# Kernel optimization log

Measured on AMD Instinct MI355X. Metric: run time of the kernel, lower is better.

The kernel has to match this reference:

```python
import jax, jax.numpy as jnp
import numpy as np

N, E = 50000, 800000
D, H, C, ED = 128, 8, 16, 4  # embed_dim, heads, head_dim, edge_dim


def _add_self_loops(edge_index, ea, n):
    # PyG add_self_loops with fill_value='mean': self-loop edge_attr is the
    # mean of incoming edge attributes per destination node (0 if none).
    src, dst = edge_index[0], edge_index[1]
    deg = jax.ops.segment_sum(jnp.ones((src.shape[0],), ea.dtype), dst, num_segments=n)
    loop_ea = jax.ops.segment_sum(ea, dst, num_segments=n) / jnp.maximum(deg, 1.0)[:, None]
    ar = jnp.arange(n, dtype=src.dtype)
    return (jnp.concatenate([src, ar]), jnp.concatenate([dst, ar]),
            jnp.concatenate([ea, loop_ea], axis=0))


def _gatv2(x, src, dst, ea, Wl, bl, Wr, br, We, att, bias, concat):
    n = x.shape[0]
    xl = (x @ Wl + bl).reshape(n, H, C)   # lin_l -> messages (source)
    xr = (x @ Wr + br).reshape(n, H, C)   # lin_r -> target
    e = (ea @ We).reshape(-1, H, C)       # lin_edge (no bias in PyG)
    m = jax.nn.leaky_relu(xl[src] + xr[dst] + e, negative_slope=0.2)  # [Etot,H,C]
    alpha = jnp.einsum('ehc,hc->eh', m, att)
    amax = jax.ops.segment_max(alpha, dst, num_segments=n)   # every node has a self loop
    ex = jnp.exp(alpha - amax[dst])
    den = jax.ops.segment_sum(ex, dst, num_segments=n)
    a = ex / den[dst]                                        # segment softmax over dst
    out = jax.ops.segment_sum(xl[src] * a[:, :, None], dst, num_segments=n)  # [N,H,C]
    out = out.reshape(n, H * C) if concat else out.mean(axis=1)
    return out + bias


def _ln(h, g, b):
    mu = h.mean(-1, keepdims=True)
    var = jnp.var(h, axis=-1, keepdims=True)
    return (h - mu) / jnp.sqrt(var + 1e-5) * g + b


def setup_inputs() -> dict:
    key = jax.random.key(0)
    ks = jax.random.split(key, 32)
    s = 0.05
    inp = {
        'x': jax.random.normal(ks[0], (N, D), jnp.float32),
        'edge_index': jax.random.randint(ks[1], (2, E), 0, N, jnp.int32),
        'edge_attr': jax.random.normal(ks[2], (E, ED), jnp.float32),
    }
    dims = [(D, H * C), (H * C, H * C), (H * C, C)]  # (in_dim, bias_dim per layer)
    k = 3
    for i, (din, bdim) in enumerate(dims):
        inp[f'Wl{i}'] = jax.random.normal(ks[k], (din, H * C), jnp.float32) * s; k += 1
        inp[f'bl{i}'] = jnp.zeros((H * C,), jnp.float32)
        inp[f'Wr{i}'] = jax.random.normal(ks[k], (din, H * C), jnp.float32) * s; k += 1
        inp[f'br{i}'] = jnp.zeros((H * C,), jnp.float32)
        inp[f'We{i}'] = jax.random.normal(ks[k], (ED, H * C), jnp.float32) * s; k += 1
        inp[f'att{i}'] = jax.random.normal(ks[k], (H, C), jnp.float32) * s; k += 1
        inp[f'b{i}'] = jnp.zeros((bdim,), jnp.float32)
        inp[f'g{i}'] = jnp.ones((bdim,), jnp.float32)
        inp[f'be{i}'] = jnp.zeros((bdim,), jnp.float32)
    inp['Wout'] = jax.random.normal(ks[k], (C, D), jnp.float32) * s
    inp['bout'] = jnp.zeros((D,), jnp.float32)
    return inp


def reference(x, edge_index, edge_attr,
              Wl0, bl0, Wr0, br0, We0, att0, b0, g0, be0,
              Wl1, bl1, Wr1, br1, We1, att1, b1, g1, be1,
              Wl2, bl2, Wr2, br2, We2, att2, b2, g2, be2,
              Wout, bout):
    n = x.shape[0]
    src, dst, ea = _add_self_loops(edge_index, edge_attr, n)
    layers = [
        (Wl0, bl0, Wr0, br0, We0, att0, b0, g0, be0, True),
        (Wl1, bl1, Wr1, br1, We1, att1, b1, g1, be1, True),
        (Wl2, bl2, Wr2, br2, We2, att2, b2, g2, be2, False),
    ]
    for (Wl, bl, Wr, br, We, att, bias, g, be, concat) in layers:
        h = _gatv2(x, src, dst, ea, Wl, bl, Wr, br, We, att, bias, concat)
        h = jax.nn.elu(h)
        h = _ln(h, g, be)
        if h.shape == x.shape:  # residual (layers 0,1)
            h = h + x
        x = h
    return x @ Wout + bout
```

## Files before the change

kernel.cpp:

```cpp
#include <hip/hip_runtime.h>
#include <hip/hip_bf16.h>

#define ND 128
#define NH 8
#define NC 16

typedef float v2f __attribute__((ext_vector_type(2)));

static inline size_t alignup(size_t x){ return (x + 255) & ~size_t(255); }

__device__ __forceinline__ ushort f2bf(float f){
    __hip_bfloat16 h = __float2bfloat16(f);
    return *reinterpret_cast<ushort*>(&h);
}

__device__ __forceinline__ v2f unpack_bf2(uint u){
    v2f r;
    r.x = __uint_as_float(u << 16);
    r.y = __uint_as_float(u & 0xffff0000u);
    return r;
}

__device__ __forceinline__ v2f lrelu2(v2f z){
    v2f s = z * 0.2f;
    v2f r;
    r.x = fmaxf(z.x, s.x);
    r.y = fmaxf(z.y, s.y);
    return r;
}

__device__ __forceinline__ float hred8(float x){
    int y;
    y = __builtin_amdgcn_mov_dpp(__float_as_int(x), 0xB1, 0xF, 0xF, true);
    x += __int_as_float(y);
    y = __builtin_amdgcn_mov_dpp(__float_as_int(x), 0x4E, 0xF, 0xF, true);
    x += __int_as_float(y);
    y = __builtin_amdgcn_mov_dpp(__float_as_int(x), 0x141, 0xF, 0xF, true);
    x += __int_as_float(y);
    return x;
}


__global__ void hist_kernel(const int* __restrict__ dsts, int* __restrict__ deg, int E)
{
    int e = blockIdx.x * blockDim.x + threadIdx.x;
    if (e >= E) return;
    atomicAdd(&deg[dsts[e]], 1);
}

__global__ __launch_bounds__(1024) void scan_kernel(const int* __restrict__ deg,
                                                    int* __restrict__ rowstart, int n)
{
    __shared__ int wsum[16];
    int tid = threadIdx.x;
    int lane = tid & 63, wid = tid >> 6;
    int carry = 0;
    for (int base = 0; base < n; base += 4096) {
        int idx = base + tid * 4;
        int4 d = make_int4(0, 0, 0, 0);
        if (idx + 3 < n) d = *(const int4*)(deg + idx);
        else {
            if (idx < n)     d.x = deg[idx];
            if (idx + 1 < n) d.y = deg[idx + 1];
            if (idx + 2 < n) d.z = deg[idx + 2];
        }
        int p0 = (d.x + 3) & ~3, p1 = (d.y + 3) & ~3;
        int p2 = (d.z + 3) & ~3, p3 = (d.w + 3) & ~3;
        int tsum = p0 + p1 + p2 + p3;
        int s = tsum;
        #pragma unroll
        for (int o = 1; o < 64; o <<= 1) {
            int t = __shfl_up(s, o);
            if (lane >= o) s += t;
        }
        if (lane == 63) wsum[wid] = s;
        __syncthreads();
        int off = carry;
        #pragma unroll
        for (int w = 0; w < 16; ++w) {
            int ws_ = wsum[w];
            if (w < wid) off += ws_;
        }
        int total = 0;
        #pragma unroll
        for (int w = 0; w < 16; ++w) total += wsum[w];
        int excl = off + (s - tsum);
        if (idx < n)     rowstart[idx]     = excl;
        if (idx + 1 < n) rowstart[idx + 1] = excl + p0;
        if (idx + 2 < n) rowstart[idx + 2] = excl + p0 + p1;
        if (idx + 3 < n) rowstart[idx + 3] = excl + p0 + p1 + p2;
        carry += total;
        __syncthreads();
    }
    if (tid == 0) rowstart[n] = carry;
}

__global__ void scatter_kernel(const int* __restrict__ srcs, const int* __restrict__ dsts,
                               const float4* __restrict__ ea4,
                               const int* __restrict__ rowstart, int* __restrict__ cursor,
                               int* __restrict__ srcb_sorted, uint2* __restrict__ eab_sorted, int E)
{
    int e = blockIdx.x * blockDim.x + threadIdx.x;
    if (e >= E) return;
    int d = dsts[e];
    int pos = rowstart[d] + atomicAdd(&cursor[d], 1);
    srcb_sorted[pos] = srcs[e] << 8;
    float4 a = ea4[e];
    uint2 p;
    p.x = (uint)f2bf(a.x) | ((uint)f2bf(a.y) << 16);
    p.y = (uint)f2bf(a.z) | ((uint)f2bf(a.w) << 16);
    eab_sorted[pos] = p;
}

__global__ void padfill_kernel(const int* __restrict__ rowstart, const int* __restrict__ deg,
                               int* __restrict__ srcb_sorted, uint2* __restrict__ eab_sorted, int n)
{
    int v = blockIdx.x * blockDim.x + threadIdx.x;
    if (v < n) {
        int d = deg[v];
        int p = rowstart[v] + d;
        int pe = rowstart[v] + ((d + 3) & ~3);
        for (; p < pe; ++p) {
            srcb_sorted[p] = 0;
            eab_sorted[p] = make_uint2(0u, 0u);
        }
    } else if (v < n + 64) {
        int p = rowstart[n] + (v - n);
        srcb_sorted[p] = 0;
        eab_sorted[p] = make_uint2(0u, 0u);
    }
}

__global__ void easum_kernel(const int* __restrict__ rowstart, const int* __restrict__ deg,
                             const uint2* __restrict__ eab_sorted, float4* __restrict__ easum, int n)
{
    int v = blockIdx.x * blockDim.x + threadIdx.x;
    if (v >= n) return;
    int p0 = rowstart[v], d = deg[v];
    float sx = 0.f, sy = 0.f, sz = 0.f, sw = 0.f;
    for (int p = p0; p < p0 + d; ++p) {
        uint2 a = eab_sorted[p];
        sx += __uint_as_float(a.x << 16);
        sy += __uint_as_float(a.x & 0xffff0000u);
        sz += __uint_as_float(a.y << 16);
        sw += __uint_as_float(a.y & 0xffff0000u);
    }
    float inv = 1.0f / (float)(d > 0 ? d : 1);
    easum[v] = make_float4(sx * inv, sy * inv, sz * inv, sw * inv);
}


__global__ __launch_bounds__(256) void gemm_xw2(const float* __restrict__ X,
                                                const float* __restrict__ Wl,
                                                const float* __restrict__ bl,
                                                const float* __restrict__ Wr,
                                                const float* __restrict__ br,
                                                ushort* __restrict__ XLB,
                                                ushort* __restrict__ XRB, int nrows)
{
    __shared__ float xs[64][128];
    __shared__ float wls[16][128];
    __shared__ float wrs[16][128];
    int tid = threadIdx.x;
    int row0 = blockIdx.x * 64;

    const float4* X4 = (const float4*)X;
    float4* xs4 = (float4*)xs;
    #pragma unroll
    for (int i = tid; i < 64*32; i += 256) {
        int r = i >> 5;
        float4 v = make_float4(0.f, 0.f, 0.f, 0.f);
        if (row0 + r < nrows) v = X4[(size_t)(row0 + r) * 32 + (i & 31)];
        xs4[i] = v;
    }

    const float4* Wl4 = (const float4*)Wl;
    const float4* Wr4 = (const float4*)Wr;
    float4 pa0 = Wl4[tid], pa1 = Wl4[tid + 256];
    float4 pb0 = Wr4[tid], pb1 = Wr4[tid + 256];

    int cg = tid & 31;
    int rg = (tid >> 5) * 8;
    v2f al0[8], al1[8], ar0[8], ar1[8];
    float4 blv = ((const float4*)bl)[cg];
    float4 brv = ((const float4*)br)[cg];
    #pragma unroll
    for (int r = 0; r < 8; r++) {
        al0[r] = (v2f){blv.x, blv.y}; al1[r] = (v2f){blv.z, blv.w};
        ar0[r] = (v2f){brv.x, brv.y}; ar1[r] = (v2f){brv.z, brv.w};
    }

    for (int kt = 0; kt < 128; kt += 16) {
        __syncthreads();
        ((float4*)wls)[tid] = pa0; ((float4*)wls)[tid + 256] = pa1;
        ((float4*)wrs)[tid] = pb0; ((float4*)wrs)[tid + 256] = pb1;
        __syncthreads();
        if (kt + 16 < 128) {
            int base = (kt + 16) * 32;
            pa0 = Wl4[base + tid]; pa1 = Wl4[base + tid + 256];
            pb0 = Wr4[base + tid]; pb1 = Wr4[base + tid + 256];
        }
        #pragma unroll
        for (int kk = 0; kk < 16; kk++) {
            float4 wl = ((const float4*)&wls[kk][0])[cg];
            float4 wr = ((const float4*)&wrs[kk][0])[cg];
            v2f wl01 = (v2f){wl.x, wl.y}, wl23 = (v2f){wl.z, wl.w};
            v2f wr01 = (v2f){wr.x, wr.y}, wr23 = (v2f){wr.z, wr.w};
            #pragma unroll
            for (int r = 0; r < 8; r++) {
                float xv = xs[rg + r][kt + kk];
                v2f xv2 = (v2f){xv, xv};
                al0[r] += xv2 * wl01;
                al1[r] += xv2 * wl23;
                ar0[r] += xv2 * wr01;
                ar1[r] += xv2 * wr23;
            }
        }
    }

    #pragma unroll
    for (int r = 0; r < 8; r++) {
        int row = row0 + rg + r;
        if (row < nrows) {
            ushort4 ol, orr;
            ol.x = f2bf(al0[r].x); ol.y = f2bf(al0[r].y);
            ol.z = f2bf(al1[r].x); ol.w = f2bf(al1[r].y);
            orr.x = f2bf(ar0[r].x); orr.y = f2bf(ar0[r].y);
            orr.z = f2bf(ar1[r].x); orr.w = f2bf(ar1[r].y);
            ((ushort4*)XLB)[(size_t)row * 32 + cg] = ol;
            ((ushort4*)XRB)[(size_t)row * 32 + cg] = orr;
        }
    }
}


__device__ __forceinline__ void gat_wave(
    int dstv, int t,
    const uint* __restrict__ xl_u, const uint* __restrict__ xr_u,
    const int* __restrict__ rowstart, const int* __restrict__ deg,
    const int* __restrict__ srcb_sorted, const uint2* __restrict__ eab_sorted,
    const float4* __restrict__ easum,
    const float* __restrict__ We, const float* __restrict__ att,
    v2f& r_out, float& l_out)
{
    v2f we0  = ((const v2f*)(We))[t];
    v2f we1  = ((const v2f*)(We + ND))[t];
    v2f we2  = ((const v2f*)(We + 2*ND))[t];
    v2f we3  = ((const v2f*)(We + 3*ND))[t];
    v2f attv = ((const v2f*)att)[t] * 1.44269504f;
    v2f xrv  = unpack_bf2(xr_u[(((uint)dstv) << 6) + t]);

    int p0 = __builtin_amdgcn_readfirstlane(rowstart[dstv]);
    int dv = __builtin_amdgcn_readfirstlane(deg[dstv]);
    int nb = (dv + 3) >> 2;

    uint xsw = xl_u[(((uint)dstv) << 6) + t];

    const int* sp = srcb_sorted + p0;
    const uint4* ebp = (const uint4*)(eab_sorted + p0);
    const char* xlc = (const char*)xl_u;
    uint t4 = (uint)t * 4u;

    v2f a = {0.f, 0.f};
    float lsum = 0.f;

    int4 s0 = *(const int4*)(sp);
    uint xA0 = *(const uint*)(xlc + ((uint)s0.x + t4));
    uint xA1 = *(const uint*)(xlc + ((uint)s0.y + t4));
    uint xA2 = *(const uint*)(xlc + ((uint)s0.z + t4));
    uint xA3 = *(const uint*)(xlc + ((uint)s0.w + t4));
    int4 s1 = *(const int4*)(sp + 4);
    uint xB0 = *(const uint*)(xlc + ((uint)s1.x + t4));
    uint xB1 = *(const uint*)(xlc + ((uint)s1.y + t4));
    uint xB2 = *(const uint*)(xlc + ((uint)s1.z + t4));
    uint xB3 = *(const uint*)(xlc + ((uint)s1.w + t4));
    int4 s2 = *(const int4*)(sp + 8);
    uint xC0 = *(const uint*)(xlc + ((uint)s2.x + t4));
    uint xC1 = *(const uint*)(xlc + ((uint)s2.y + t4));
    uint xC2 = *(const uint*)(xlc + ((uint)s2.z + t4));
    uint xC3 = *(const uint*)(xlc + ((uint)s2.w + t4));
    int4 s3 = *(const int4*)(sp + 12);
    uint4 eA = ebp[0];
    uint4 eB = ebp[1];

    for (int ib = 0; ib < nb; ++ib) {
        uint xD0 = *(const uint*)(xlc + ((uint)s3.x + t4));
        uint xD1 = *(const uint*)(xlc + ((uint)s3.y + t4));
        uint xD2 = *(const uint*)(xlc + ((uint)s3.z + t4));
        uint xD3 = *(const uint*)(xlc + ((uint)s3.w + t4));
        int4 s4 = *(const int4*)(sp + ib*4 + 16);
        uint4 eNA = ebp[(ib + 1) * 2];
        uint4 eNB = ebp[(ib + 1) * 2 + 1];

        float e0x = __uint_as_float(eA.x << 16), e0y = __uint_as_float(eA.x & 0xffff0000u);
        float e0z = __uint_as_float(eA.y << 16), e0w = __uint_as_float(eA.y & 0xffff0000u);
        float e1x = __uint_as_float(eA.z << 16), e1y = __uint_as_float(eA.z & 0xffff0000u);
        float e1z = __uint_as_float(eA.w << 16), e1w = __uint_as_float(eA.w & 0xffff0000u);
        float e2x = __uint_as_float(eB.x << 16), e2y = __uint_as_float(eB.x & 0xffff0000u);
        float e2z = __uint_as_float(eB.y << 16), e2w = __uint_as_float(eB.y & 0xffff0000u);
        float e3x = __uint_as_float(eB.z << 16), e3y = __uint_as_float(eB.z & 0xffff0000u);
        float e3z = __uint_as_float(eB.w << 16), e3w = __uint_as_float(eB.w & 0xffff0000u);

        v2f b0 = xrv + we0*e0x + we1*e0y + we2*e0z + we3*e0w;
        v2f b1 = xrv + we0*e1x + we1*e1y + we2*e1z + we3*e1w;
        v2f b2 = xrv + we0*e2x + we1*e2y + we2*e2z + we3*e2w;
        v2f b3 = xrv + we0*e3x + we1*e3y + we2*e3z + we3*e3w;

        v2f x0 = unpack_bf2(xA0);
        v2f x1 = unpack_bf2(xA1);
        v2f x2 = unpack_bf2(xA2);
        v2f x3 = unpack_bf2(xA3);

        v2f l0 = lrelu2(x0 + b0);
        v2f l1 = lrelu2(x1 + b1);
        v2f l2 = lrelu2(x2 + b2);
        v2f l3 = lrelu2(x3 + b3);

        v2f q0 = l0 * attv;
        v2f q1 = l1 * attv;
        v2f q2 = l2 * attv;
        v2f q3 = l3 * attv;
        float pt0 = q0.x + q0.y;
        float pt1 = q1.x + q1.y;
        float pt2 = q2.x + q2.y;
        float pt3 = q3.x + q3.y;

        if (ib == nb - 1) {
            int live = dv - ib*4;
            pt1 = (live > 1) ? pt1 : -1e30f;
            pt2 = (live > 2) ? pt2 : -1e30f;
            pt3 = (live > 3) ? pt3 : -1e30f;
        }

        float al0 = hred8(pt0);
        float al1 = hred8(pt1);
        float al2 = hred8(pt2);
        float al3 = hred8(pt3);

        float pe0 = exp2f(al0);
        float pe1 = exp2f(al1);
        float pe2 = exp2f(al2);
        float pe3 = exp2f(al3);
        lsum += (pe0 + pe1) + (pe2 + pe3);
        a += x0 * pe0;
        a += x1 * pe1;
        a += x2 * pe2;
        a += x3 * pe3;

        xA0 = xB0; xA1 = xB1; xA2 = xB2; xA3 = xB3;
        xB0 = xC0; xB1 = xC1; xB2 = xC2; xB3 = xC3;
        xC0 = xD0; xC1 = xD1; xC2 = xD2; xC3 = xD3;
        s3 = s4;
        eA = eNA; eB = eNB;
    }

    float4 em = easum[dstv];
    v2f xs = unpack_bf2(xsw);
    v2f bs = xrv + we0*em.x + we1*em.y + we2*em.z + we3*em.w;
    v2f ls = lrelu2(xs + bs);
    v2f qs = ls * attv;
    float al = hred8(qs.x + qs.y);
    float pe = exp2f(al);
    l_out = lsum + pe;
    r_out = a + xs * pe;
}

__global__ __launch_bounds__(256) void attn_concat(
    const ushort* __restrict__ xlb, const ushort* __restrict__ xrb,
    const float* __restrict__ xin,
    const int* __restrict__ rowstart, const int* __restrict__ deg,
    const int* __restrict__ srcb_sorted, const uint2* __restrict__ eab_sorted,
    const float4* __restrict__ easum,
    const float* __restrict__ We, const float* __restrict__ att,
    const float* __restrict__ bias, const float* __restrict__ g, const float* __restrict__ be,
    float* __restrict__ out, int n)
{
    int wid = threadIdx.x >> 6;
    int t = threadIdx.x & 63;
    int dstv = blockIdx.x * 4 + wid;
    if (dstv >= n) return;

    v2f av; float l;
    gat_wave(dstv, t, (const uint*)xlb, (const uint*)xrb, rowstart, deg, srcb_sorted,
             eab_sorted, easum, We, att, av, l);

    v2f bv = ((const v2f*)bias)[t];
    float linv = 1.0f / l;
    v2f h = av * linv + bv;
    h.x = h.x > 0.f ? h.x : (__expf(h.x) - 1.0f);
    h.y = h.y > 0.f ? h.y : (__expf(h.y) - 1.0f);

    float ss = h.x + h.y, qq = h.x*h.x + h.y*h.y;
    #pragma unroll
    for (int o = 1; o < 64; o <<= 1) { ss += __shfl_xor(ss, o); qq += __shfl_xor(qq, o); }
    float mu = ss * (1.0f / ND);
    float var = qq * (1.0f / ND) - mu * mu;
    float rstd = rsqrtf(var + 1e-5f);

    v2f gv  = ((const v2f*)g)[t];
    v2f bev = ((const v2f*)be)[t];
    v2f xiv = ((const v2f*)(xin + (size_t)dstv * ND))[t];
    v2f o2 = (h - mu) * rstd * gv + bev + xiv;
    ((v2f*)(out + (size_t)dstv * ND))[t] = o2;
}

__global__ __launch_bounds__(256) void attn_final(
    const ushort* __restrict__ xlb, const ushort* __restrict__ xrb,
    const int* __restrict__ rowstart, const int* __restrict__ deg,
    const int* __restrict__ srcb_sorted, const uint2* __restrict__ eab_sorted,
    const float4* __restrict__ easum,
    const float* __restrict__ We, const float* __restrict__ att,
    const float* __restrict__ b2, const float* __restrict__ g2, const float* __restrict__ be2,
    const float* __restrict__ Wout, const float* __restrict__ bout,
    float* __restrict__ out, int n)
{
    __shared__ float h16s[4][16];
    int wid = threadIdx.x >> 6;
    int t = threadIdx.x & 63;
    int dstv = blockIdx.x * 4 + wid;
    if (dstv >= n) return;

    v2f av; float l;
    gat_wave(dstv, t, (const uint*)xlb, (const uint*)xrb, rowstart, deg, srcb_sorted,
             eab_sorted, easum, We, att, av, l);
    float linv = 1.0f / l;
    float v0 = av.x * linv, v1 = av.y * linv;

    #pragma unroll
    for (int o = 8; o < 64; o <<= 1) { v0 += __shfl_xor(v0, o); v1 += __shfl_xor(v1, o); }
    int cc = t & 7;
    float2 b2v = ((const float2*)b2)[cc];
    v0 = v0 * (1.0f / NH) + b2v.x;
    v1 = v1 * (1.0f / NH) + b2v.y;
    v0 = v0 > 0.f ? v0 : (__expf(v0) - 1.0f);
    v1 = v1 > 0.f ? v1 : (__expf(v1) - 1.0f);

    float ss = v0 + v1, qq = v0*v0 + v1*v1;
    #pragma unroll
    for (int o = 1; o < 8; o <<= 1) { ss += __shfl_xor(ss, o); qq += __shfl_xor(qq, o); }
    float mu = ss * (1.0f / NC);
    float var = qq * (1.0f / NC) - mu * mu;
    float rstd = rsqrtf(var + 1e-5f);
    float2 g2v = ((const float2*)g2)[cc];
    float2 be2v = ((const float2*)be2)[cc];
    float t0 = (v0 - mu) * rstd * g2v.x + be2v.x;
    float t1 = (v1 - mu) * rstd * g2v.y + be2v.y;

    if (t < 8) { h16s[wid][2*t] = t0; h16s[wid][2*t + 1] = t1; }

    float2 ov = ((const float2*)bout)[t];
    #pragma unroll
    for (int k = 0; k < NC; k++) {
        float hk = h16s[wid][k];
        float2 wv = ((const float2*)Wout)[k * 64 + t];
        ov.x = fmaf(hk, wv.x, ov.x);
        ov.y = fmaf(hk, wv.y, ov.y);
    }
    ((float2*)(out + (size_t)dstv * ND))[t] = ov;
}


extern "C" void kernel_launch(void* const* d_in, const int* in_sizes, int n_in,
                              void* d_out, int out_size, void* d_ws, size_t ws_size,
                              hipStream_t stream)
{
    const float* x_in = (const float*)d_in[0];
    const int*   ei   = (const int*)d_in[1];
    const float* ea   = (const float*)d_in[2];
    const int N = in_sizes[0] / ND;
    const int E = in_sizes[1] / 2;
    const int* srcs = ei;
    const int* dsts = ei + E;
    const float4* ea4 = (const float4*)ea;

    const float *Wl[3], *bl[3], *Wr[3], *br[3], *We[3], *att[3], *bb[3], *gg[3], *be[3];
    for (int l = 0; l < 3; l++) {
        int b = 3 + 9 * l;
        Wl[l]  = (const float*)d_in[b + 0];
        bl[l]  = (const float*)d_in[b + 1];
        Wr[l]  = (const float*)d_in[b + 2];
        br[l]  = (const float*)d_in[b + 3];
        We[l]  = (const float*)d_in[b + 4];
        att[l] = (const float*)d_in[b + 5];
        bb[l]  = (const float*)d_in[b + 6];
        gg[l]  = (const float*)d_in[b + 7];
        be[l]  = (const float*)d_in[b + 8];
    }
    const float* Wout = (const float*)d_in[30];
    const float* bout = (const float*)d_in[31];

    const size_t EP = (size_t)E + 3 * (size_t)N + 96;

    char* ws = (char*)d_ws;
    size_t off = 0;
    int* deg        = (int*)(ws + off);      off = alignup(off + (size_t)N * 4);
    int* cursor     = (int*)(ws + off);      off = alignup(off + (size_t)N * 4);
    size_t zero_bytes = off;
    int* rowstart   = (int*)(ws + off);      off = alignup(off + (size_t)(N + 1) * 4);
    int* srcb_sorted = (int*)(ws + off);     off = alignup(off + EP * 4);
    uint2* eab_sorted = (uint2*)(ws + off);  off = alignup(off + EP * 8);
    float4* easum   = (float4*)(ws + off);   off = alignup(off + (size_t)N * 16);
    ushort* xlb     = (ushort*)(ws + off);   off = alignup(off + (size_t)N * ND * 2);
    ushort* xrb     = (ushort*)(ws + off);   off = alignup(off + (size_t)N * ND * 2);
    float* xa       = (float*)(ws + off);    off = alignup(off + (size_t)N * ND * 4);
    float* xb       = (float*)d_out;

    hipMemsetAsync(d_ws, 0, zero_bytes, stream);

    int ethreads = 256;
    int eblocks = (E + ethreads - 1) / ethreads;
    hist_kernel<<<eblocks, ethreads, 0, stream>>>(dsts, deg, E);
    scan_kernel<<<1, 1024, 0, stream>>>(deg, rowstart, N);
    padfill_kernel<<<(N + 64 + 255) / 256, 256, 0, stream>>>(rowstart, deg, srcb_sorted, eab_sorted, N);
    scatter_kernel<<<eblocks, ethreads, 0, stream>>>(srcs, dsts, ea4, rowstart, cursor,
                                                     srcb_sorted, eab_sorted, E);
    easum_kernel<<<(N + 255) / 256, 256, 0, stream>>>(rowstart, deg, eab_sorted, easum, N);

    int gblocks = (N + 63) / 64;
    int ablocks = (N + 3) / 4;

    gemm_xw2<<<gblocks, 256, 0, stream>>>(x_in, Wl[0], bl[0], Wr[0], br[0], xlb, xrb, N);
    attn_concat<<<ablocks, 256, 0, stream>>>(xlb, xrb, x_in, rowstart, deg, srcb_sorted, eab_sorted,
                                             easum, We[0], att[0], bb[0], gg[0], be[0], xa, N);
    gemm_xw2<<<gblocks, 256, 0, stream>>>(xa, Wl[1], bl[1], Wr[1], br[1], xlb, xrb, N);
    attn_concat<<<ablocks, 256, 0, stream>>>(xlb, xrb, xa, rowstart, deg, srcb_sorted, eab_sorted,
                                             easum, We[1], att[1], bb[1], gg[1], be[1], xb, N);
    gemm_xw2<<<gblocks, 256, 0, stream>>>(xb, Wl[2], bl[2], Wr[2], br[2], xlb, xrb, N);
    attn_final<<<ablocks, 256, 0, stream>>>(xlb, xrb, rowstart, deg, srcb_sorted, eab_sorted,
                                            easum, We[2], att[2], bb[2], gg[2], be[2],
                                            Wout, bout, (float*)d_out, N);
}
```

Baseline: 459.5 us.

## Replace FP32 FMA projection GEMM with split-bf16 MFMA kernel

```diff
diff --git a/kernel.cpp b/kernel.cpp
--- a/kernel.cpp
+++ b/kernel.cpp
@@ -6,6 +6,8 @@
 #define NC 16
 
 typedef float v2f __attribute__((ext_vector_type(2)));
+typedef short bf16x8 __attribute__((ext_vector_type(8)));
+typedef float f32x4 __attribute__((ext_vector_type(4)));
 
 static inline size_t alignup(size_t x){ return (x + 255) & ~size_t(255); }
 
@@ -150,85 +152,91 @@
 }
 
 
-__global__ __launch_bounds__(256) void gemm_xw2(const float* __restrict__ X,
-                                                const float* __restrict__ Wl,
-                                                const float* __restrict__ bl,
-                                                const float* __restrict__ Wr,
-                                                const float* __restrict__ br,
-                                                ushort* __restrict__ XLB,
-                                                ushort* __restrict__ XRB, int nrows)
-{
-    __shared__ float xs[64][128];
-    __shared__ float wls[16][128];
-    __shared__ float wrs[16][128];
+struct WSrc { const float* p[6]; };
+
+__global__ void wconv_kernel(WSrc s, ushort* __restrict__ wt)
+{
+    int id = blockIdx.x * blockDim.x + threadIdx.x;
+    int m = id >> 14;
+    int r = id & 16383;
+    int n = r >> 7, k = r & 127;
+    wt[(size_t)m * 16384 + n * 128 + k] = f2bf(s.p[m][k * 128 + n]);
+}
+
+
+__global__ __launch_bounds__(256) void gemm_mfma(
+    const float* __restrict__ X,
+    const ushort* __restrict__ WTl, const float* __restrict__ bl,
+    const ushort* __restrict__ WTr, const float* __restrict__ br,
+    ushort* __restrict__ XLB, ushort* __restrict__ XRB, int nrows)
+{
+    __shared__ ushort xhi[64][136];
+    __shared__ ushort xlo[64][136];
     int tid = threadIdx.x;
     int row0 = blockIdx.x * 64;
 
     const float4* X4 = (const float4*)X;
-    float4* xs4 = (float4*)xs;
     #pragma unroll
     for (int i = tid; i < 64*32; i += 256) {
-        int r = i >> 5;
+        int r = i >> 5, c = i & 31;
         float4 v = make_float4(0.f, 0.f, 0.f, 0.f);
-        if (row0 + r < nrows) v = X4[(size_t)(row0 + r) * 32 + (i & 31)];
-        xs4[i] = v;
-    }
-
-    const float4* Wl4 = (const float4*)Wl;
-    const float4* Wr4 = (const float4*)Wr;
-    float4 pa0 = Wl4[tid], pa1 = Wl4[tid + 256];
-    float4 pb0 = Wr4[tid], pb1 = Wr4[tid + 256];
-
-    int cg = tid & 31;
-    int rg = (tid >> 5) * 8;
-    v2f al0[8], al1[8], ar0[8], ar1[8];
-    float4 blv = ((const float4*)bl)[cg];
-    float4 brv = ((const float4*)br)[cg];
-    #pragma unroll
-    for (int r = 0; r < 8; r++) {
-        al0[r] = (v2f){blv.x, blv.y}; al1[r] = (v2f){blv.z, blv.w};
-        ar0[r] = (v2f){brv.x, brv.y}; ar1[r] = (v2f){brv.z, brv.w};
-    }
-
-    for (int kt = 0; kt < 128; kt += 16) {
-        __syncthreads();
-        ((float4*)wls)[tid] = pa0; ((float4*)wls)[tid + 256] = pa1;
-        ((float4*)wrs)[tid] = pb0; ((float4*)wrs)[tid + 256] = pb1;
-        __syncthreads();
-        if (kt + 16 < 128) {
-            int base = (kt + 16) * 32;
-            pa0 = Wl4[base + tid]; pa1 = Wl4[base + tid + 256];
-            pb0 = Wr4[base + tid]; pb1 = Wr4[base + tid + 256];
-        }
+        if (row0 + r < nrows) v = X4[(size_t)(row0 + r) * 32 + c];
+        ushort4 h, l;
+        h.x = f2bf(v.x); l.x = f2bf(v.x - __uint_as_float((uint)h.x << 16));
+        h.y = f2bf(v.y); l.y = f2bf(v.y - __uint_as_float((uint)h.y << 16));
+        h.z = f2bf(v.z); l.z = f2bf(v.z - __uint_as_float((uint)h.z << 16));
+        h.w = f2bf(v.w); l.w = f2bf(v.w - __uint_as_float((uint)h.w << 16));
+        *(ushort4*)&xhi[r][c * 4] = h;
+        *(ushort4*)&xlo[r][c * 4] = l;
+    }
+    __syncthreads();
+
+    int lane = tid & 63;
+    int wid = tid >> 6;
+    int c15 = lane & 15;
+    int kblk = lane >> 4;
+    int rowb = wid * 16;
+
+    f32x4 accl[8], accr[8];
+    #pragma unroll
+    for (int nt = 0; nt < 8; ++nt) {
+        float bvl = bl[nt * 16 + c15];
+        float bvr = br[nt * 16 + c15];
+        accl[nt] = (f32x4){bvl, bvl, bvl, bvl};
+        accr[nt] = (f32x4){bvr, bvr, bvr, bvr};
+    }
+
+    const bf16x8* WL8 = (const bf16x8*)WTl;
+    const bf16x8* WR8 = (const bf16x8*)WTr;
+
+    #pragma unroll
+    for (int kc = 0; kc < 4; ++kc) {
+        int k0 = kc * 32 + kblk * 8;
+        bf16x8 ahi = *(const bf16x8*)&xhi[rowb + c15][k0];
+        bf16x8 alo = *(const bf16x8*)&xlo[rowb + c15][k0];
+        int kidx = k0 >> 3;
         #pragma unroll
-        for (int kk = 0; kk < 16; kk++) {
-            float4 wl = ((const float4*)&wls[kk][0])[cg];
-            float4 wr = ((const float4*)&wrs[kk][0])[cg];
-            v2f wl01 = (v2f){wl.x, wl.y}, wl23 = (v2f){wl.z, wl.w};
-            v2f wr01 = (v2f){wr.x, wr.y}, wr23 = (v2f){wr.z, wr.w};
+        for (int nt = 0; nt < 8; ++nt) {
+            int bi = (nt * 16 + c15) * 16 + kidx;
+            bf16x8 bfl = WL8[bi];
+            bf16x8 bfr = WR8[bi];
+            accl[nt] = __builtin_amdgcn_mfma_f32_16x16x32_bf16(ahi, bfl, accl[nt], 0, 0, 0);
+            accl[nt] = __builtin_amdgcn_mfma_f32_16x16x32_bf16(alo, bfl, accl[nt], 0, 0, 0);
+            accr[nt] = __builtin_amdgcn_mfma_f32_16x16x32_bf16(ahi, bfr, accr[nt], 0, 0, 0);
+            accr[nt] = __builtin_amdgcn_mfma_f32_16x16x32_bf16(alo, bfr, accr[nt], 0, 0, 0);
+        }
+    }
+
+    int crow = rowb + (lane >> 4) * 4;
+    #pragma unroll
+    for (int j = 0; j < 4; ++j) {
+        int row = row0 + crow + j;
+        if (row < nrows) {
             #pragma unroll
-            for (int r = 0; r < 8; r++) {
-                float xv = xs[rg + r][kt + kk];
-                v2f xv2 = (v2f){xv, xv};
-                al0[r] += xv2 * wl01;
-                al1[r] += xv2 * wl23;
-                ar0[r] += xv2 * wr01;
-                ar1[r] += xv2 * wr23;
+            for (int nt = 0; nt < 8; ++nt) {
+                XLB[(size_t)row * 128 + nt * 16 + c15] = f2bf(accl[nt][j]);
+                XRB[(size_t)row * 128 + nt * 16 + c15] = f2bf(accr[nt][j]);
             }
-        }
-    }
-
-    #pragma unroll
-    for (int r = 0; r < 8; r++) {
-        int row = row0 + rg + r;
-        if (row < nrows) {
-            ushort4 ol, orr;
-            ol.x = f2bf(al0[r].x); ol.y = f2bf(al0[r].y);
-            ol.z = f2bf(al1[r].x); ol.w = f2bf(al1[r].y);
-            orr.x = f2bf(ar0[r].x); orr.y = f2bf(ar0[r].y);
-            orr.z = f2bf(ar1[r].x); orr.w = f2bf(ar1[r].y);
-            ((ushort4*)XLB)[(size_t)row * 32 + cg] = ol;
-            ((ushort4*)XRB)[(size_t)row * 32 + cg] = orr;
         }
     }
 }
@@ -503,9 +511,16 @@
     ushort* xlb     = (ushort*)(ws + off);   off = alignup(off + (size_t)N * ND * 2);
     ushort* xrb     = (ushort*)(ws + off);   off = alignup(off + (size_t)N * ND * 2);
     float* xa       = (float*)(ws + off);    off = alignup(off + (size_t)N * ND * 4);
+    ushort* wt      = (ushort*)(ws + off);   off = alignup(off + (size_t)6 * 16384 * 2);
     float* xb       = (float*)d_out;
 
     hipMemsetAsync(d_ws, 0, zero_bytes, stream);
+
+    WSrc wsrc;
+    wsrc.p[0] = Wl[0]; wsrc.p[1] = Wr[0];
+    wsrc.p[2] = Wl[1]; wsrc.p[3] = Wr[1];
+    wsrc.p[4] = Wl[2]; wsrc.p[5] = Wr[2];
+    wconv_kernel<<<(6 * 16384) / 256, 256, 0, stream>>>(wsrc, wt);
 
     int ethreads = 256;
     int eblocks = (E + ethreads - 1) / ethreads;
@@ -519,13 +534,20 @@
     int gblocks = (N + 63) / 64;
     int ablocks = (N + 3) / 4;
 
-    gemm_xw2<<<gblocks, 256, 0, stream>>>(x_in, Wl[0], bl[0], Wr[0], br[0], xlb, xrb, N);
+    const ushort* WT0l = wt;
+    const ushort* WT0r = wt + 16384;
+    const ushort* WT1l = wt + 2 * 16384;
+    const ushort* WT1r = wt + 3 * 16384;
+    const ushort* WT2l = wt + 4 * 16384;
+    const ushort* WT2r = wt + 5 * 16384;
+
+    gemm_mfma<<<gblocks, 256, 0, stream>>>(x_in, WT0l, bl[0], WT0r, br[0], xlb, xrb, N);
     attn_concat<<<ablocks, 256, 0, stream>>>(xlb, xrb, x_in, rowstart, deg, srcb_sorted, eab_sorted,
                                              easum, We[0], att[0], bb[0], gg[0], be[0], xa, N);
-    gemm_xw2<<<gblocks, 256, 0, stream>>>(xa, Wl[1], bl[1], Wr[1], br[1], xlb, xrb, N);
+    gemm_mfma<<<gblocks, 256, 0, stream>>>(xa, WT1l, bl[1], WT1r, br[1], xlb, xrb, N);
     attn_concat<<<ablocks, 256, 0, stream>>>(xlb, xrb, xa, rowstart, deg, srcb_sorted, eab_sorted,
                                              easum, We[1], att[1], bb[1], gg[1], be[1], xb, N);
-    gemm_xw2<<<gblocks, 256, 0, stream>>>(xb, Wl[2], bl[2], Wr[2], br[2], xlb, xrb, N);
+    gemm_mfma<<<gblocks, 256, 0, stream>>>(xb, WT2l, bl[2], WT2r, br[2], xlb, xrb, N);
     attn_final<<<ablocks, 256, 0, stream>>>(xlb, xrb, rowstart, deg, srcb_sorted, eab_sorted,
                                             easum, We[2], att[2], bb[2], gg[2], be[2],
                                             Wout, bout, (float*)d_out, N);
```

Result: faster. 420.0 us (-8.6%).
